# Performance work log

Hardware: AMD Instinct MI355X
Metric: run time of the kernel (lower is better)

The kernel has to match this reference:

```python
import jax, jax.numpy as jnp
import numpy as np

B, E, P, BIT = 2048, 512, 4096, 64
H, HD, HID = 8, 64, 4096


def _l2norm(x, eps=1e-12):
    n = jnp.sqrt(jnp.sum(x * x, axis=1, keepdims=True))
    return x / jnp.maximum(n, eps)


def _mha(q, k, v, in_w, in_b, out_w, out_b):
    # torch.nn.MultiheadAttention, unbatched 2D input [L, E]
    qp = q @ in_w[:E].T + in_b[:E]
    kp = k @ in_w[E:2 * E].T + in_b[E:2 * E]
    vp = v @ in_w[2 * E:].T + in_b[2 * E:]
    L, S = q.shape[0], k.shape[0]
    qh = qp.reshape(L, H, HD).transpose(1, 0, 2)   # [H, L, HD]
    kh = kp.reshape(S, H, HD).transpose(1, 0, 2)
    vh = vp.reshape(S, H, HD).transpose(1, 0, 2)
    scores = jnp.einsum('hld,hsd->hls', qh, kh) / jnp.sqrt(jnp.float32(HD))
    attn = jax.nn.softmax(scores, axis=-1)
    out = jnp.einsum('hls,hsd->hld', attn, vh).transpose(1, 0, 2).reshape(L, E)
    return out @ out_w.T + out_b


def _mlp(x, W1, b1, W2, b2, Wc, bc):
    h = jax.nn.relu(x @ W1.T + b1)
    h = jax.nn.relu(h @ W2.T + b2)
    return _l2norm(h @ Wc.T + bc)


def setup_inputs():
    key = jax.random.key(0)
    ks = jax.random.split(key, 24)
    s = 0.02
    inp = {
        'image_feature': jax.random.normal(ks[0], (B, E), dtype=jnp.float32),
        'text_feature': jax.random.normal(ks[1], (B, E), dtype=jnp.float32),
        'prompts': jax.random.normal(ks[2], (P, E), dtype=jnp.float32),
        'img_in_w': jax.random.normal(ks[3], (3 * E, E), dtype=jnp.float32) * s,
        'img_in_b': jnp.zeros((3 * E,), jnp.float32),
        'img_out_w': jax.random.normal(ks[4], (E, E), dtype=jnp.float32) * s,
        'img_out_b': jnp.zeros((E,), jnp.float32),
        'txt_in_w': jax.random.normal(ks[5], (3 * E, E), dtype=jnp.float32) * s,
        'txt_in_b': jnp.zeros((3 * E,), jnp.float32),
        'txt_out_w': jax.random.normal(ks[6], (E, E), dtype=jnp.float32) * s,
        'txt_out_b': jnp.zeros((E,), jnp.float32),
        'img_W1': jax.random.normal(ks[7], (HID, 2 * E), dtype=jnp.float32) * s,
        'img_b1': jnp.zeros((HID,), jnp.float32),
        'img_W2': jax.random.normal(ks[8], (HID, HID), dtype=jnp.float32) * s,
        'img_b2': jnp.zeros((HID,), jnp.float32),
        'img_Wc': jax.random.normal(ks[9], (BIT, HID), dtype=jnp.float32) * s,
        'img_bc': jnp.zeros((BIT,), jnp.float32),
        'txt_W1': jax.random.normal(ks[10], (HID, 2 * E), dtype=jnp.float32) * s,
        'txt_b1': jnp.zeros((HID,), jnp.float32),
        'txt_W2': jax.random.normal(ks[11], (HID, HID), dtype=jnp.float32) * s,
        'txt_b2': jnp.zeros((HID,), jnp.float32),
        'txt_Wc': jax.random.normal(ks[12], (BIT, HID), dtype=jnp.float32) * s,
        'txt_bc': jnp.zeros((BIT,), jnp.float32),
        'iteration': 0,
    }
    return inp


def reference(image_feature, text_feature, prompts,
              img_in_w, img_in_b, img_out_w, img_out_b,
              txt_in_w, txt_in_b, txt_out_w, txt_out_b,
              img_W1, img_b1, img_W2, img_b2, img_Wc, img_bc,
              txt_W1, txt_b1, txt_W2, txt_b2, txt_Wc, txt_bc,
              iteration):
    # prompt_mode == 'share': cosine-sim matmul + argmax nearest-prompt + gather
    idx_i = jnp.argmax(image_feature @ prompts.T, axis=1)
    idx_t = jnp.argmax(text_feature @ prompts.T, axis=1)
    rm_i = prompts[idx_i]  # [B, E]
    rm_t = prompts[idx_t]
    enh_i = _mha(image_feature, rm_i, rm_i, img_in_w, img_in_b, img_out_w, img_out_b)
    enh_t = _mha(text_feature, rm_t, rm_t, txt_in_w, txt_in_b, txt_out_w, txt_out_b)
    fi = jnp.concatenate([image_feature, enh_i], axis=1)  # [B, 2E]
    ft = jnp.concatenate([text_feature, enh_t], axis=1)
    distill_i = _mlp(ft, img_W1, img_b1, img_W2, img_b2, img_Wc, img_bc)
    distill_t = _mlp(fi, txt_W1, txt_b1, txt_W2, txt_b2, txt_Wc, txt_bc)
    image_hash = _mlp(fi, img_W1, img_b1, img_W2, img_b2, img_Wc, img_bc)
    text_hash = _mlp(ft, txt_W1, txt_b1, txt_W2, txt_b2, txt_Wc, txt_bc)
    return (image_hash, text_hash, distill_i, distill_t)
```

## Files before the change

### kernel.cpp

```cpp
#include <hip/hip_runtime.h>
#include <cstdint>
#include <cstddef>

typedef _Float16 F16;
typedef _Float16 f16x8 __attribute__((ext_vector_type(8)));
typedef float f32x4 __attribute__((ext_vector_type(4)));

#define ASYNC_COPY16(gsrc, ldst)                                                        \
  __builtin_amdgcn_global_load_lds((const __attribute__((address_space(1))) void*)(gsrc), \
                                   (__attribute__((address_space(3))) void*)(ldst), 16, 0, 0)

constexpr int NCAST = 11;
struct CastJobs {
  const float* src[NCAST];
  F16* dst[NCAST];
  int nblk[NCAST];
};

__global__ __launch_bounds__(256) void cast_many(CastJobs j) {
  int rem = blockIdx.x;
  const float* src = j.src[0];
  F16* dst = j.dst[0];
  bool found = false;
#pragma unroll
  for (int s = 0; s < NCAST; ++s) {
    bool here = !found && (rem < j.nblk[s]);
    if (here) { src = j.src[s]; dst = j.dst[s]; found = true; }
    if (!found) rem -= j.nblk[s];
  }
  size_t i = ((size_t)rem * 256 + threadIdx.x) * 8;
  float4 a = *(const float4*)&src[i];
  float4 b = *(const float4*)&src[i + 4];
  f16x8 o;
  o[0] = (F16)a.x; o[1] = (F16)a.y; o[2] = (F16)a.z; o[3] = (F16)a.w;
  o[4] = (F16)b.x; o[5] = (F16)b.y; o[6] = (F16)b.z; o[7] = (F16)b.w;
  *(f16x8*)&dst[i] = o;
}

__global__ __launch_bounds__(256) void cast_one(const float* __restrict__ in,
                                                F16* __restrict__ out) {
  size_t i = ((size_t)blockIdx.x * 256 + threadIdx.x) * 8;
  float4 a = *(const float4*)&in[i];
  float4 b = *(const float4*)&in[i + 4];
  f16x8 o;
  o[0] = (F16)a.x; o[1] = (F16)a.y; o[2] = (F16)a.z; o[3] = (F16)a.w;
  o[4] = (F16)b.x; o[5] = (F16)b.y; o[6] = (F16)b.z; o[7] = (F16)b.w;
  *(f16x8*)&out[i] = o;
}

__global__ __launch_bounds__(256) void cast_half_cols(const float* __restrict__ src_i,
                                                      const float* __restrict__ src_t,
                                                      F16* __restrict__ fi, F16* __restrict__ ft) {
  int mod = blockIdx.z;
  const float* in = mod ? src_t : src_i;
  F16* out = mod ? ft : fi;
  int t = blockIdx.x * 256 + threadIdx.x;
  int i = t * 8;
  int row = i >> 9, c = i & 511;
  float4 a = *(const float4*)&in[(size_t)row * 512 + c];
  float4 b = *(const float4*)&in[(size_t)row * 512 + c + 4];
  f16x8 o;
  o[0] = (F16)a.x; o[1] = (F16)a.y; o[2] = (F16)a.z; o[3] = (F16)a.w;
  o[4] = (F16)b.x; o[5] = (F16)b.y; o[6] = (F16)b.z; o[7] = (F16)b.w;
  *(f16x8*)&out[(size_t)row * 1024 + c] = o;
}

__global__ __launch_bounds__(256) void argmax_part(const float* __restrict__ feat_i,
                                                   const float* __restrict__ feat_t,
                                                   const float* __restrict__ prompts,
                                                   float* __restrict__ pval, int* __restrict__ pidx) {
  const int mod = blockIdx.z;
  const float* feat = mod ? feat_t : feat_i;
  const int r0 = blockIdx.x * 64;
  const int p0 = blockIdx.y * 128;
  const int tid = threadIdx.x;
  const int tx = tid & 15, ty = tid >> 4;
  __shared__ __align__(16) float sA[64][36];
  __shared__ __align__(16) float sB[128][36];
  float acc[4][8] = {};
  for (int kt = 0; kt < 512; kt += 32) {
#pragma unroll
    for (int i = 0; i < 2; ++i) {
      int t = tid + 256 * i;
      int row = t >> 3, c = (t & 7) * 4;
      *(float4*)&sA[row][c] = *(const float4*)&feat[(size_t)(r0 + row) * 512 + kt + c];
    }
#pragma unroll
    for (int i = 0; i < 4; ++i) {
      int t = tid + 256 * i;
      int row = t >> 3, c = (t & 7) * 4;
      *(float4*)&sB[row][c] = *(const float4*)&prompts[(size_t)(p0 + row) * 512 + kt + c];
    }
    __syncthreads();
#pragma unroll
    for (int k = 0; k < 32; k += 4) {
      float4 a[4];
#pragma unroll
      for (int i = 0; i < 4; ++i) a[i] = *(const float4*)&sA[ty * 4 + i][k];
#pragma unroll
      for (int jj = 0; jj < 8; ++jj) {
        float4 b = *(const float4*)&sB[jj * 16 + tx][k];
#pragma unroll
        for (int i = 0; i < 4; ++i) {
          acc[i][jj] = fmaf(a[i].x, b.x, acc[i][jj]);
          acc[i][jj] = fmaf(a[i].y, b.y, acc[i][jj]);
          acc[i][jj] = fmaf(a[i].z, b.z, acc[i][jj]);
          acc[i][jj] = fmaf(a[i].w, b.w, acc[i][jj]);
        }
      }
    }
    __syncthreads();
  }
#pragma unroll
  for (int i = 0; i < 4; ++i) {
    float v = acc[i][0];
    int id = p0 + tx;
#pragma unroll
    for (int jj = 1; jj < 8; ++jj) {
      int idx = p0 + jj * 16 + tx;
      if (acc[i][jj] > v) { v = acc[i][jj]; id = idx; }
    }
#pragma unroll
    for (int off = 1; off < 16; off <<= 1) {
      float ov = __shfl_xor(v, off);
      int oi = __shfl_xor(id, off);
      if (ov > v || (ov == v && oi < id)) { v = ov; id = oi; }
    }
    if (tx == 0) {
      pval[((size_t)mod * 2048 + r0 + ty * 4 + i) * 32 + blockIdx.y] = v;
      pidx[((size_t)mod * 2048 + r0 + ty * 4 + i) * 32 + blockIdx.y] = id;
    }
  }
}

__global__ __launch_bounds__(256) void argmax_merge_gather(const float* __restrict__ pval,
                                                           const int* __restrict__ pidx,
                                                           const F16* __restrict__ prompts_h,
                                                           F16* __restrict__ rm_i,
                                                           F16* __restrict__ rm_t) {
  int tid = threadIdx.x;
  int w = tid >> 6, lane = tid & 63;
  int rowg = blockIdx.x * 4 + w;
  int mod = rowg >> 11, r = rowg & 2047;
  const float* pv = pval + ((size_t)mod * 2048 + r) * 32;
  const int* pi = pidx + ((size_t)mod * 2048 + r) * 32;
  float v = (lane < 32) ? pv[lane] : -3.4e38f;
  int id = (lane < 32) ? pi[lane] : 0x7fffffff;
#pragma unroll
  for (int off = 16; off; off >>= 1) {
    float ov = __shfl_down(v, off);
    int oi = __shfl_down(id, off);
    if (ov > v || (ov == v && oi < id)) { v = ov; id = oi; }
  }
  int bid = __shfl(id, 0);
  const F16* src = prompts_h + (size_t)bid * 512;
  F16* dst = (mod ? rm_t : rm_i) + (size_t)r * 512;
  *(f16x8*)(dst + lane * 8) = *(const f16x8*)(src + lane * 8);
}

struct Ptrs8 {
  const F16* A[8];
  const F16* B[8];
  const float* bias[8];
  void* D[8];
};

template <int BM, int BN, int WM, int WN, int ACT, int OUTF32, int L2N = 0>
__global__ __launch_bounds__(256) void gemm_nt(Ptrs8 p, int K, int lda, int ldb, int ldd) {
  constexpr int SM = BM / WM, SN = BN / WN;
  constexpr int FM = SM / 16, FN = SN / 16;
  __shared__ __align__(16) F16 sA[BM * 32];
  __shared__ __align__(16) F16 sB[BN * 32];
  const int tid = threadIdx.x;
  const int lane = tid & 63, wid = tid >> 6;
  const int wr = wid / WN, wc = wid % WN;
  const int z = blockIdx.z;
  const F16* A = p.A[z] + (size_t)blockIdx.x * BM * lda;
  const F16* B = p.B[z] + (size_t)blockIdx.y * BN * ldb;

  f32x4 acc[FM][FN] = {};

  const int kfrag = (lane >> 4) * 8;
  const int rA = wr * SM + (lane & 15);
  const int rB = wc * SN + (lane & 15);

  for (int kt = 0; kt < K; kt += 32) {
#pragma unroll
    for (int i = 0; i < (BM * 4) / 256; ++i) {
      int t = tid + 256 * i;
      int row = t >> 2, c = t & 3;
      ASYNC_COPY16(A + (size_t)row * lda + kt + c * 8, sA + t * 8);
    }
#pragma unroll
    for (int i = 0; i < (BN * 4) / 256; ++i) {
      int t = tid + 256 * i;
      int row = t >> 2, c = t & 3;
      ASYNC_COPY16(B + (size_t)row * ldb + kt + c * 8, sB + t * 8);
    }
    __syncthreads();
    f16x8 af[FM], bf[FN];
#pragma unroll
    for (int m = 0; m < FM; ++m) af[m] = *(const f16x8*)&sA[(rA + m * 16) * 32 + kfrag];
#pragma unroll
    for (int n = 0; n < FN; ++n) bf[n] = *(const f16x8*)&sB[(rB + n * 16) * 32 + kfrag];
#pragma unroll
    for (int m = 0; m < FM; ++m)
#pragma unroll
      for (int n = 0; n < FN; ++n)
        acc[m][n] = __builtin_amdgcn_mfma_f32_16x16x32_f16(af[m], bf[n], acc[m][n], 0, 0, 0);
    __syncthreads();
  }

  const float* bias = p.bias[z];
  if constexpr (L2N) {
    __shared__ float sOut[64][68];
#pragma unroll
    for (int m = 0; m < FM; ++m)
#pragma unroll
      for (int n = 0; n < FN; ++n) {
        int c = wc * SN + n * 16 + (lane & 15);
        float bv = bias[c];
#pragma unroll
        for (int jj = 0; jj < 4; ++jj) {
          int r = wr * SM + m * 16 + (lane >> 4) * 4 + jj;
          sOut[r][c] = acc[m][n][jj] + bv;
        }
      }
    __syncthreads();
    int row = tid >> 2, q = tid & 3;
    float4 xv[4];
    float s = 0.f;
#pragma unroll
    for (int c4 = 0; c4 < 4; ++c4) {
      xv[c4] = *(const float4*)&sOut[row][q * 16 + c4 * 4];
      s += xv[c4].x * xv[c4].x + xv[c4].y * xv[c4].y + xv[c4].z * xv[c4].z + xv[c4].w * xv[c4].w;
    }
    s += __shfl_xor(s, 1);
    s += __shfl_xor(s, 2);
    float inv = 1.f / fmaxf(sqrtf(s), 1e-12f);
    float* D = (float*)p.D[z] + (size_t)(blockIdx.x * BM + row) * 64 + q * 16;
#pragma unroll
    for (int c4 = 0; c4 < 4; ++c4) {
      float4 o;
      o.x = xv[c4].x * inv; o.y = xv[c4].y * inv; o.z = xv[c4].z * inv; o.w = xv[c4].w * inv;
      *(float4*)&D[c4 * 4] = o;
    }
  } else {
    const int m0 = blockIdx.x * BM + wr * SM, n0 = blockIdx.y * BN + wc * SN;
#pragma unroll
    for (int m = 0; m < FM; ++m) {
#pragma unroll
      for (int n = 0; n < FN; ++n) {
        int col = n0 + n * 16 + (lane & 15);
        float bv = bias ? bias[col] : 0.f;
#pragma unroll
        for (int jj = 0; jj < 4; ++jj) {
          int row = m0 + m * 16 + (lane >> 4) * 4 + jj;
          float v = acc[m][n][jj] + bv;
          if (ACT) v = fmaxf(v, 0.f);
          if (OUTF32)
            ((float*)p.D[z])[(size_t)row * ldd + col] = v;
          else
            ((F16*)p.D[z])[(size_t)row * ldd + col] = (F16)v;
        }
      }
    }
  }
}

__global__ __launch_bounds__(256) void softmax_rows(F16* __restrict__ s) {
  const size_t row = blockIdx.x;
  F16* p = s + row * 2048;
  const int tid = threadIdx.x;
  const int w = tid >> 6, lane = tid & 63;
  f16x8 v8 = *(const f16x8*)(p + tid * 8);
  float v[8];
#pragma unroll
  for (int j = 0; j < 8; ++j) v[j] = (float)v8[j];
  float m = -3.4e38f;
#pragma unroll
  for (int j = 0; j < 8; ++j) m = fmaxf(m, v[j]);
#pragma unroll
  for (int off = 32; off; off >>= 1) m = fmaxf(m, __shfl_xor(m, off));
  __shared__ float red[8];
  if (lane == 0) red[w] = m;
  __syncthreads();
  m = fmaxf(fmaxf(red[0], red[1]), fmaxf(red[2], red[3]));
  float sum = 0.f;
#pragma unroll
  for (int j = 0; j < 8; ++j) {
    v[j] = __expf((v[j] - m) * 0.125f);
    sum += v[j];
  }
#pragma unroll
  for (int off = 32; off; off >>= 1) sum += __shfl_xor(sum, off);
  if (lane == 0) red[4 + w] = sum;
  __syncthreads();
  sum = red[4] + red[5] + red[6] + red[7];
  float inv = 1.f / sum;
  f16x8 o;
#pragma unroll
  for (int j = 0; j < 8; ++j) o[j] = (F16)(v[j] * inv);
  *(f16x8*)(p + tid * 8) = o;
}

__global__ __launch_bounds__(256) void transpose_vp(const F16* __restrict__ qkv_i,
                                                    const F16* __restrict__ qkv_t,
                                                    F16* __restrict__ vpT_i, F16* __restrict__ vpT_t) {
  int mod = blockIdx.z;
  const F16* vp = (mod ? qkv_t : qkv_i) + 1024;
  F16* vpT = mod ? vpT_t : vpT_i;
  int s0 = blockIdx.x * 64, d0 = blockIdx.y * 64;
  __shared__ __align__(16) F16 tile[64][72];
  int tid = threadIdx.x;
#pragma unroll
  for (int i = 0; i < 2; ++i) {
    int ch = tid + 256 * i;
    int row = ch >> 3, c = (ch & 7) * 8;
    *(f16x8*)&tile[row][c] = *(const f16x8*)&vp[(size_t)(s0 + row) * 1536 + d0 + c];
  }
  __syncthreads();
#pragma unroll
  for (int i = 0; i < 2; ++i) {
    int ch = tid + 256 * i;
    int dr = ch >> 3, sc = (ch & 7) * 8;
    f16x8 o;
#pragma unroll
    for (int j = 0; j < 8; ++j) o[j] = tile[sc + j][dr];
    *(f16x8*)&vpT[(size_t)(d0 + dr) * 2048 + s0 + sc] = o;
  }
}

extern "C" void kernel_launch(void* const* d_in, const int* in_sizes, int n_in, void* d_out,
                              int out_size, void* d_ws, size_t ws_size, hipStream_t stream) {
  const float* img_f = (const float*)d_in[0];
  const float* txt_f = (const float*)d_in[1];
  const float* prompts = (const float*)d_in[2];
  const float* img_in_w = (const float*)d_in[3];
  const float* img_in_b = (const float*)d_in[4];
  const float* img_out_w = (const float*)d_in[5];
  const float* img_out_b = (const float*)d_in[6];
  const float* txt_in_w = (const float*)d_in[7];
  const float* txt_in_b = (const float*)d_in[8];
  const float* txt_out_w = (const float*)d_in[9];
  const float* txt_out_b = (const float*)d_in[10];
  const float* img_W1 = (const float*)d_in[11];
  const float* img_b1 = (const float*)d_in[12];
  const float* img_W2 = (const float*)d_in[13];
  const float* img_b2 = (const float*)d_in[14];
  const float* img_Wc = (const float*)d_in[15];
  const float* img_bc = (const float*)d_in[16];
  const float* txt_W1 = (const float*)d_in[17];
  const float* txt_b1 = (const float*)d_in[18];
  const float* txt_W2 = (const float*)d_in[19];
  const float* txt_b2 = (const float*)d_in[20];
  const float* txt_Wc = (const float*)d_in[21];
  const float* txt_bc = (const float*)d_in[22];
  float* out = (float*)d_out;

  char* ws = (char*)d_ws;
  size_t off = 0;
  auto alloc = [&](size_t bytes) -> void* {
    void* p = ws + off;
    off += (bytes + 255) & ~(size_t)255;
    return p;
  };
  F16* prompts_h = (F16*)alloc((size_t)4096 * 512 * 2);
  F16* in_w_i_h = (F16*)alloc((size_t)1536 * 512 * 2);
  F16* in_w_t_h = (F16*)alloc((size_t)1536 * 512 * 2);
  F16* out_w_i_h = (F16*)alloc((size_t)512 * 512 * 2);
  F16* out_w_t_h = (F16*)alloc((size_t)512 * 512 * 2);
  F16* W1_i = (F16*)alloc((size_t)4096 * 1024 * 2);
  F16* W1_t = (F16*)alloc((size_t)4096 * 1024 * 2);
  F16* Wc_i = (F16*)alloc((size_t)64 * 4096 * 2);
  F16* Wc_t = (F16*)alloc((size_t)64 * 4096 * 2);
  float* pval = (float*)alloc((size_t)2 * 2048 * 32 * 4);
  int* pidx = (int*)alloc((size_t)2 * 2048 * 32 * 4);
  F16* rm_i = (F16*)alloc((size_t)2048 * 512 * 2);
  F16* rm_t = (F16*)alloc((size_t)2048 * 512 * 2);
  F16* qkv_i = (F16*)alloc((size_t)2048 * 1536 * 2);
  F16* qkv_t = (F16*)alloc((size_t)2048 * 1536 * 2);
  F16* vpT_i = (F16*)alloc((size_t)512 * 2048 * 2);
  F16* vpT_t = (F16*)alloc((size_t)512 * 2048 * 2);
  F16* attn_i = (F16*)alloc((size_t)2048 * 512 * 2);
  F16* attn_t = (F16*)alloc((size_t)2048 * 512 * 2);
  F16* fi = (F16*)alloc((size_t)2048 * 1024 * 2);
  F16* ft = (F16*)alloc((size_t)2048 * 1024 * 2);
  F16* scores = (F16*)alloc((size_t)8 * 2048 * 2048 * 2);

  const size_t W2B = (size_t)4096 * 4096 * 2;
  const size_t H2B = (size_t)4 * 2048 * 4096 * 2;
  F16 *W2_i = nullptr, *W2_t = nullptr, *W2_shared = nullptr, *h2full = nullptr;
  int zb;
  if (off + 2 * W2B + H2B <= ws_size) {
    W2_i = (F16*)alloc(W2B); W2_t = (F16*)alloc(W2B); h2full = (F16*)alloc(H2B); zb = 4;
  } else if (off + 2 * W2B <= ws_size) {
    W2_i = (F16*)alloc(W2B); W2_t = (F16*)alloc(W2B); zb = 2;
  } else if (off + W2B <= ws_size) {
    W2_shared = (F16*)alloc(W2B); zb = 2;
  } else {
    return;
  }

  {
    CastJobs j;
    const int w2blk = W2_i ? 8192 : 0;
    const float* srcs[NCAST] = {img_W2, txt_W2, img_W1, txt_W1, prompts,
                                img_in_w, txt_in_w, img_out_w, txt_out_w, img_Wc, txt_Wc};
    F16* dsts[NCAST] = {W2_i ? W2_i : W2_shared, W2_t ? W2_t : W2_shared, W1_i, W1_t, prompts_h,
                        in_w_i_h, in_w_t_h, out_w_i_h, out_w_t_h, Wc_i, Wc_t};
    const int nb[NCAST] = {w2blk, w2blk, 2048, 2048, 1024, 384, 384, 128, 128, 128, 128};
    int total = 0;
    for (int s = 0; s < NCAST; ++s) { j.src[s] = srcs[s]; j.dst[s] = dsts[s]; j.nblk[s] = nb[s]; total += nb[s]; }
    cast_many<<<dim3(total), 256, 0, stream>>>(j);
  }
  cast_half_cols<<<dim3(512, 1, 2), 256, 0, stream>>>(img_f, txt_f, fi, ft);

  argmax_part<<<dim3(32, 32, 2), 256, 0, stream>>>(img_f, txt_f, prompts, pval, pidx);
  argmax_merge_gather<<<dim3(1024), 256, 0, stream>>>(pval, pidx, prompts_h, rm_i, rm_t);

  {
    Ptrs8 p{};
    p.A[0] = fi; p.B[0] = in_w_i_h; p.bias[0] = img_in_b; p.D[0] = qkv_i;
    p.A[1] = ft; p.B[1] = in_w_t_h; p.bias[1] = txt_in_b; p.D[1] = qkv_t;
    gemm_nt<128, 128, 2, 2, 0, 0><<<dim3(16, 4, 2), 256, 0, stream>>>(p, 512, 1024, 512, 1536);
  }
  {
    Ptrs8 p{};
    p.A[0] = rm_i; p.B[0] = in_w_i_h + (size_t)512 * 512; p.bias[0] = img_in_b + 512; p.D[0] = qkv_i + 512;
    p.A[1] = rm_t; p.B[1] = in_w_t_h + (size_t)512 * 512; p.bias[1] = txt_in_b + 512; p.D[1] = qkv_t + 512;
    gemm_nt<128, 128, 2, 2, 0, 0><<<dim3(16, 8, 2), 256, 0, stream>>>(p, 512, 512, 512, 1536);
  }
  transpose_vp<<<dim3(32, 8, 2), 256, 0, stream>>>(qkv_i, qkv_t, vpT_i, vpT_t);

  for (int mod = 0; mod < 2; ++mod) {
    F16* qkv = mod ? qkv_t : qkv_i;
    F16* vpT = mod ? vpT_t : vpT_i;
    F16* attn = mod ? attn_t : attn_i;
    {
      Ptrs8 p{};
      for (int h = 0; h < 8; ++h) {
        p.A[h] = qkv + h * 64;
        p.B[h] = qkv + 512 + h * 64;
        p.bias[h] = nullptr;
        p.D[h] = scores + (size_t)h * 2048 * 2048;
      }
      gemm_nt<128, 128, 2, 2, 0, 0><<<dim3(16, 16, 8), 256, 0, stream>>>(p, 64, 1536, 1536, 2048);
    }
    softmax_rows<<<dim3(16384), 256, 0, stream>>>(scores);
    {
      Ptrs8 p{};
      for (int h = 0; h < 8; ++h) {
        p.A[h] = scores + (size_t)h * 2048 * 2048;
        p.B[h] = vpT + (size_t)h * 64 * 2048;
        p.bias[h] = nullptr;
        p.D[h] = attn + h * 64;
      }
      gemm_nt<64, 64, 2, 2, 0, 0><<<dim3(32, 1, 8), 256, 0, stream>>>(p, 2048, 2048, 2048, 512);
    }
  }
  {
    Ptrs8 p{};
    p.A[0] = attn_i; p.B[0] = out_w_i_h; p.bias[0] = img_out_b; p.D[0] = fi + 512;
    p.A[1] = attn_t; p.B[1] = out_w_t_h; p.bias[1] = txt_out_b; p.D[1] = ft + 512;
    gemm_nt<128, 128, 2, 2, 0, 0><<<dim3(16, 4, 2), 256, 0, stream>>>(p, 512, 512, 512, 1024);
  }

  const int zlist[4] = {0, 2, 1, 3};
  const F16* mlpA[4] = {fi, ft, ft, fi};
  const float* mb1[4] = {img_b1, txt_b1, img_b1, txt_b1};
  const float* mb2[4] = {img_b2, txt_b2, img_b2, txt_b2};
  const float* mbc[4] = {img_bc, txt_bc, img_bc, txt_bc};
  const F16* mW1[4] = {W1_i, W1_t, W1_i, W1_t};
  const F16* mWc[4] = {Wc_i, Wc_t, Wc_i, Wc_t};

  for (int b0 = 0; b0 < 4; b0 += zb) {
    F16* h1 = scores;
    F16* h2 = h2full ? h2full : scores + (size_t)zb * 2048 * 4096;
    {
      Ptrs8 p{};
      for (int q = 0; q < zb; ++q) {
        int z = zlist[b0 + q];
        p.A[q] = mlpA[z]; p.B[q] = mW1[z]; p.bias[q] = mb1[z];
        p.D[q] = h1 + (size_t)q * 2048 * 4096;
      }
      gemm_nt<128, 128, 2, 2, 1, 0><<<dim3(16, 32, zb), 256, 0, stream>>>(p, 1024, 1024, 1024, 4096);
    }
    {
      const F16* w2a = nullptr, *w2b = nullptr;
      if (W2_i) {
        w2a = (zlist[b0] == 0 || zlist[b0] == 2) ? W2_i : W2_t;
        w2b = (zb == 4) ? nullptr : w2a;
      } else {
        const float* srcw2 = (zlist[b0] == 0 || zlist[b0] == 2) ? img_W2 : txt_W2;
        cast_one<<<dim3(8192), 256, 0, stream>>>(srcw2, W2_shared);
        w2a = W2_shared;
      }
      Ptrs8 p{};
      for (int q = 0; q < zb; ++q) {
        int z = zlist[b0 + q];
        const F16* wz = W2_i ? ((z == 0 || z == 2) ? W2_i : W2_t) : w2a;
        p.A[q] = h1 + (size_t)q * 2048 * 4096; p.B[q] = wz; p.bias[q] = mb2[z];
        p.D[q] = h2 + (size_t)q * 2048 * 4096;
      }
      (void)w2b;
      gemm_nt<128, 128, 2, 2, 1, 0><<<dim3(16, 32, zb), 256, 0, stream>>>(p, 4096, 4096, 4096, 4096);
    }
    {
      Ptrs8 p{};
      for (int q = 0; q < zb; ++q) {
        int z = zlist[b0 + q];
        p.A[q] = h2 + (size_t)q * 2048 * 4096; p.B[q] = mWc[z]; p.bias[q] = mbc[z];
        p.D[q] = out + (size_t)z * 2048 * 64;
      }
      gemm_nt<64, 64, 2, 2, 0, 1, 1><<<dim3(32, 1, zb), 256, 0, stream>>>(p, 4096, 4096, 4096, 64);
    }
  }
}
```

Measured before the change: 1.240 ms.

## Split-K the Wc projection, swizzle LDS layout, and remap workgroup order

Adds a KSPLIT template mode so the final Wc GEMM (K=4096, only 32 blocks per batch) splits K into four partial-sum slices written as fp32. A new reduce kernel sums the slices, adds the bias and applies the L2 norm. Separately, the LDS tile layout is XOR-swizzled on both the copy and fragment-read sides to cut bank conflicts. Block IDs are also remapped across 8-way groups, likely to spread work over XCDs and improve L2 locality. The trade-off is an extra partial buffer, an extra kernel launch, and a changed block-to-tile mapping that affects every GEMM.

```diff
diff --git a/kernel.cpp b/kernel.cpp
--- a/kernel.cpp
+++ b/kernel.cpp
@@ -165,7 +165,7 @@
   void* D[8];
 };
 
-template <int BM, int BN, int WM, int WN, int ACT, int OUTF32, int L2N = 0>
+template <int BM, int BN, int WM, int WN, int ACT, int OUTF32, int L2N = 0, int KSPLIT = 1>
 __global__ __launch_bounds__(256) void gemm_nt(Ptrs8 p, int K, int lda, int ldb, int ldd) {
   constexpr int SM = BM / WM, SN = BN / WN;
   constexpr int FM = SM / 16, FN = SN / 16;
@@ -174,35 +174,48 @@
   const int tid = threadIdx.x;
   const int lane = tid & 63, wid = tid >> 6;
   const int wr = wid / WN, wc = wid % WN;
-  const int z = blockIdx.z;
-  const F16* A = p.A[z] + (size_t)blockIdx.x * BM * lda;
-  const F16* B = p.B[z] + (size_t)blockIdx.y * BN * ldb;
+
+  const int gx = gridDim.x, gy = gridDim.y;
+  const int nwg = gx * gy * gridDim.z;
+  int id = blockIdx.x + gx * (blockIdx.y + gy * blockIdx.z);
+  id = (id & 7) * (nwg >> 3) + (id >> 3);
+  const int bx = id % gx;
+  const int tq = id / gx;
+  const int by = tq % gy;
+  const int bz = tq / gy;
+
+  const F16* A = p.A[bz] + (size_t)bx * BM * lda;
+  const F16* B = p.B[bz] + (KSPLIT > 1 ? (size_t)0 : (size_t)by * BN * ldb);
+  const int k0 = (KSPLIT > 1) ? by * K : 0;
 
   f32x4 acc[FM][FN] = {};
 
   const int kfrag = (lane >> 4) * 8;
+  const int kfx = kfrag ^ ((((lane & 15) >> 1) & 3) << 3);
   const int rA = wr * SM + (lane & 15);
   const int rB = wc * SN + (lane & 15);
 
-  for (int kt = 0; kt < K; kt += 32) {
+  for (int kt = k0; kt < k0 + K; kt += 32) {
 #pragma unroll
     for (int i = 0; i < (BM * 4) / 256; ++i) {
       int t = tid + 256 * i;
-      int row = t >> 2, c = t & 3;
-      ASYNC_COPY16(A + (size_t)row * lda + kt + c * 8, sA + t * 8);
+      int row = t >> 2;
+      int c8 = (t & 3) ^ ((t >> 3) & 3);
+      ASYNC_COPY16(A + (size_t)row * lda + kt + c8 * 8, sA + t * 8);
     }
 #pragma unroll
     for (int i = 0; i < (BN * 4) / 256; ++i) {
       int t = tid + 256 * i;
-      int row = t >> 2, c = t & 3;
-      ASYNC_COPY16(B + (size_t)row * ldb + kt + c * 8, sB + t * 8);
+      int row = t >> 2;
+      int c8 = (t & 3) ^ ((t >> 3) & 3);
+      ASYNC_COPY16(B + (size_t)row * ldb + kt + c8 * 8, sB + t * 8);
     }
     __syncthreads();
     f16x8 af[FM], bf[FN];
 #pragma unroll
-    for (int m = 0; m < FM; ++m) af[m] = *(const f16x8*)&sA[(rA + m * 16) * 32 + kfrag];
-#pragma unroll
-    for (int n = 0; n < FN; ++n) bf[n] = *(const f16x8*)&sB[(rB + n * 16) * 32 + kfrag];
+    for (int m = 0; m < FM; ++m) af[m] = *(const f16x8*)&sA[(rA + m * 16) * 32 + kfx];
+#pragma unroll
+    for (int n = 0; n < FN; ++n) bf[n] = *(const f16x8*)&sB[(rB + n * 16) * 32 + kfx];
 #pragma unroll
     for (int m = 0; m < FM; ++m)
 #pragma unroll
@@ -211,7 +224,7 @@
     __syncthreads();
   }
 
-  const float* bias = p.bias[z];
+  const float* bias = p.bias[bz];
   if constexpr (L2N) {
     __shared__ float sOut[64][68];
 #pragma unroll
@@ -238,7 +251,7 @@
     s += __shfl_xor(s, 1);
     s += __shfl_xor(s, 2);
     float inv = 1.f / fmaxf(sqrtf(s), 1e-12f);
-    float* D = (float*)p.D[z] + (size_t)(blockIdx.x * BM + row) * 64 + q * 16;
+    float* D = (float*)p.D[bz] + (size_t)(bx * BM + row) * 64 + q * 16;
 #pragma unroll
     for (int c4 = 0; c4 < 4; ++c4) {
       float4 o;
@@ -246,26 +259,47 @@
       *(float4*)&D[c4 * 4] = o;
     }
   } else {
-    const int m0 = blockIdx.x * BM + wr * SM, n0 = blockIdx.y * BN + wc * SN;
+    const int m0 = bx * BM + wr * SM;
+    const int n0 = (KSPLIT > 1 ? 0 : by * BN) + wc * SN;
+    float* Dks = nullptr;
+    if (OUTF32)
+      Dks = (float*)p.D[bz] + (KSPLIT > 1 ? (size_t)by * gx * BM * 64 : (size_t)0);
 #pragma unroll
     for (int m = 0; m < FM; ++m) {
 #pragma unroll
       for (int n = 0; n < FN; ++n) {
         int col = n0 + n * 16 + (lane & 15);
-        float bv = bias ? bias[col] : 0.f;
+        float bv = (KSPLIT > 1 || !bias) ? 0.f : bias[col];
 #pragma unroll
         for (int jj = 0; jj < 4; ++jj) {
           int row = m0 + m * 16 + (lane >> 4) * 4 + jj;
           float v = acc[m][n][jj] + bv;
           if (ACT) v = fmaxf(v, 0.f);
           if (OUTF32)
-            ((float*)p.D[z])[(size_t)row * ldd + col] = v;
+            Dks[(size_t)row * ldd + col] = v;
           else
-            ((F16*)p.D[z])[(size_t)row * ldd + col] = (F16)v;
+            ((F16*)p.D[bz])[(size_t)row * ldd + col] = (F16)v;
         }
       }
     }
   }
+}
+
+__global__ __launch_bounds__(256) void reduce_l2norm(const float* __restrict__ part,
+                                                     const float* __restrict__ bci,
+                                                     const float* __restrict__ bct,
+                                                     float* __restrict__ out) {
+  int tid = threadIdx.x;
+  int w = tid >> 6, lane = tid & 63;
+  int rowg = blockIdx.x * 4 + w;
+  int z = rowg >> 11, r = rowg & 2047;
+  const float* pz = part + (((size_t)z * 4) * 2048 + r) * 64 + lane;
+  float x = pz[0] + pz[(size_t)2048 * 64] + pz[(size_t)2 * 2048 * 64] + pz[(size_t)3 * 2048 * 64];
+  x += ((z == 0 || z == 2) ? bci : bct)[lane];
+  float s = x * x;
+#pragma unroll
+  for (int off = 32; off; off >>= 1) s += __shfl_xor(s, off);
+  out[((size_t)z * 2048 + r) * 64 + lane] = x / fmaxf(sqrtf(s), 1e-12f);
 }
 
 __global__ __launch_bounds__(256) void softmax_rows(F16* __restrict__ s) {
@@ -386,6 +420,7 @@
   F16* attn_t = (F16*)alloc((size_t)2048 * 512 * 2);
   F16* fi = (F16*)alloc((size_t)2048 * 1024 * 2);
   F16* ft = (F16*)alloc((size_t)2048 * 1024 * 2);
+  float* wc_part = (float*)alloc((size_t)4 * 4 * 2048 * 64 * 4);
   F16* scores = (F16*)alloc((size_t)8 * 2048 * 2048 * 2);
 
   const size_t W2B = (size_t)4096 * 4096 * 2;
@@ -470,7 +505,6 @@
   const F16* mlpA[4] = {fi, ft, ft, fi};
   const float* mb1[4] = {img_b1, txt_b1, img_b1, txt_b1};
   const float* mb2[4] = {img_b2, txt_b2, img_b2, txt_b2};
-  const float* mbc[4] = {img_bc, txt_bc, img_bc, txt_bc};
   const F16* mW1[4] = {W1_i, W1_t, W1_i, W1_t};
   const F16* mWc[4] = {Wc_i, Wc_t, Wc_i, Wc_t};
 
@@ -487,33 +521,28 @@
       gemm_nt<128, 128, 2, 2, 1, 0><<<dim3(16, 32, zb), 256, 0, stream>>>(p, 1024, 1024, 1024, 4096);
     }
     {
-      const F16* w2a = nullptr, *w2b = nullptr;
-      if (W2_i) {
-        w2a = (zlist[b0] == 0 || zlist[b0] == 2) ? W2_i : W2_t;
-        w2b = (zb == 4) ? nullptr : w2a;
-      } else {
+      if (!W2_i) {
         const float* srcw2 = (zlist[b0] == 0 || zlist[b0] == 2) ? img_W2 : txt_W2;
         cast_one<<<dim3(8192), 256, 0, stream>>>(srcw2, W2_shared);
-        w2a = W2_shared;
       }
       Ptrs8 p{};
       for (int q = 0; q < zb; ++q) {
         int z = zlist[b0 + q];
-        const F16* wz = W2_i ? ((z == 0 || z == 2) ? W2_i : W2_t) : w2a;
+        const F16* wz = W2_i ? ((z == 0 || z == 2) ? W2_i : W2_t) : W2_shared;
         p.A[q] = h1 + (size_t)q * 2048 * 4096; p.B[q] = wz; p.bias[q] = mb2[z];
         p.D[q] = h2 + (size_t)q * 2048 * 4096;
       }
-      (void)w2b;
       gemm_nt<128, 128, 2, 2, 1, 0><<<dim3(16, 32, zb), 256, 0, stream>>>(p, 4096, 4096, 4096, 4096);
     }
     {
       Ptrs8 p{};
       for (int q = 0; q < zb; ++q) {
         int z = zlist[b0 + q];
-        p.A[q] = h2 + (size_t)q * 2048 * 4096; p.B[q] = mWc[z]; p.bias[q] = mbc[z];
-        p.D[q] = out + (size_t)z * 2048 * 64;
-      }
-      gemm_nt<64, 64, 2, 2, 0, 1, 1><<<dim3(32, 1, zb), 256, 0, stream>>>(p, 4096, 4096, 4096, 64);
-    }
-  }
-}
+        p.A[q] = h2 + (size_t)q * 2048 * 4096; p.B[q] = mWc[z]; p.bias[q] = nullptr;
+        p.D[q] = wc_part + (size_t)z * 4 * 2048 * 64;
+      }
+      gemm_nt<64, 64, 2, 2, 0, 1, 0, 4><<<dim3(32, 4, zb), 256, 0, stream>>>(p, 1024, 4096, 4096, 64);
+    }
+  }
+  reduce_l2norm<<<dim3(2048), 256, 0, stream>>>(wc_part, img_bc, txt_bc, out);
+}
```

After: 1.268 ms. +2.2%, slower.
